# Kernel optimization log

Measured on AMD Instinct MI355X. Metric: run time of the kernel, lower is better.

Reference implementation:

```python
import jax, jax.numpy as jnp
import numpy as np


def setup_inputs() -> dict:
    key = jax.random.key(0)
    k1, k2, k3, k4 = jax.random.split(key, 4)
    B, Q, D, H = 8, 512, 4096, 1024
    return {
        "query_embeddings": jax.random.normal(k1, (B, Q, H), dtype=jnp.float32),
        "document_embeddings": jax.random.normal(k2, (B, D, H), dtype=jnp.float32),
        "attention_mask": jax.random.randint(k3, (B, D), 0, 2, dtype=jnp.int32),
        "proj_w": jax.random.normal(k4, (H, H), dtype=jnp.float32) * (H ** -0.5),
        "proj_b": jnp.zeros((H,), dtype=jnp.float32),
    }


def reference(query_embeddings, document_embeddings, attention_mask, proj_w, proj_b):
    H = query_embeddings.shape[-1]
    scale = 1.0 / jnp.sqrt(jnp.asarray(H, dtype=query_embeddings.dtype))
    # Linear projection of queries: [B, Q, H]
    q = jnp.einsum("bqh,hk->bqk", query_embeddings, proj_w) + proj_b
    # Scores: [B, Q, D]
    scores = jnp.einsum("bqh,bdh->bqd", q, document_embeddings) * scale
    # Mask: [B, 1, D]; masked positions -> -inf before softmax
    mask = attention_mask[:, None, :] != 0
    scores = jnp.where(mask, scores, -jnp.inf)
    attention_weights = jax.nn.softmax(scores, axis=-1)
    # Weighted sum over docs: [B, Q, H]
    retrieved_docs = jnp.einsum("bqd,bdh->bqh", attention_weights, document_embeddings)
    return (retrieved_docs, attention_weights)
```

## Files before the change

### kernel.cpp

```cpp
#include <hip/hip_runtime.h>

#define BATCH 8
#define QLEN 512
#define DLEN 4096
#define HDIM 1024

typedef __attribute__((ext_vector_type(8))) short bf16x8;
typedef __attribute__((ext_vector_type(4))) float f32x4;
typedef __attribute__((ext_vector_type(4))) short s16x4;

__device__ __forceinline__ short f2bf(float f) {
    union { float f; unsigned u; } x; x.f = f;
    unsigned r = x.u + 0x7fffu + ((x.u >> 16) & 1u);
    return (short)(r >> 16);
}

__device__ __forceinline__ void gload_lds16(const void* g, void* l) {
    __builtin_amdgcn_global_load_lds(
        (const __attribute__((address_space(1))) unsigned int*)g,
        (__attribute__((address_space(3))) unsigned int*)l,
        16, 0, 0);
}

__global__ void cvt_f32_bf16(const float* __restrict__ in, short* __restrict__ out, int n4) {
    int i = blockIdx.x * blockDim.x + threadIdx.x;
    int stride = gridDim.x * blockDim.x;
    for (; i < n4; i += stride) {
        float4 x = ((const float4*)in)[i];
        s16x4 o = { f2bf(x.x), f2bf(x.y), f2bf(x.z), f2bf(x.w) };
        ((s16x4*)out)[i] = o;
    }
}

__global__ void transpose_w(const float* __restrict__ W, short* __restrict__ Wt) {
    __shared__ float t[32][33];
    const int hb = blockIdx.y * 32, kb = blockIdx.x * 32;
    #pragma unroll
    for (int i = 0; i < 4; ++i) {
        int h = threadIdx.y + i * 8;
        t[h][threadIdx.x] = W[(size_t)(hb + h) * HDIM + kb + threadIdx.x];
    }
    __syncthreads();
    #pragma unroll
    for (int i = 0; i < 4; ++i) {
        int k = threadIdx.y + i * 8;
        Wt[(size_t)(kb + k) * HDIM + hb + threadIdx.x] = f2bf(t[threadIdx.x][k]);
    }
}

__global__ void transpose_docs(const short* __restrict__ docsB, short* __restrict__ docsT) {
    __shared__ unsigned t[64][65];
    const int b = blockIdx.z;
    const int h0 = blockIdx.x * 64, d0 = blockIdx.y * 64;
    const int tq = threadIdx.x & 15;
    const int tr = threadIdx.x >> 4;
    #pragma unroll
    for (int i = 0; i < 4; ++i) {
        int d = tr + i * 16;
        s16x4 v = *(const s16x4*)(docsB + ((size_t)b * DLEN + d0 + d) * HDIM + h0 + tq * 4);
        t[d][tq * 4 + 0] = (unsigned short)v[0];
        t[d][tq * 4 + 1] = (unsigned short)v[1];
        t[d][tq * 4 + 2] = (unsigned short)v[2];
        t[d][tq * 4 + 3] = (unsigned short)v[3];
    }
    __syncthreads();
    #pragma unroll
    for (int i = 0; i < 4; ++i) {
        int h = tr + i * 16;
        s16x4 o = { (short)t[tq * 4 + 0][h], (short)t[tq * 4 + 1][h],
                    (short)t[tq * 4 + 2][h], (short)t[tq * 4 + 3][h] };
        *(s16x4*)(docsT + ((size_t)b * HDIM + h0 + h) * DLEN + d0 + tq * 4) = o;
    }
}

#define BM 128
#define BN 128
#define BK 64
#define TILE_SH (BM * BK)

template<int EPI>
__global__ void gemm_bt(const short* __restrict__ A, const short* __restrict__ B,
                        void* __restrict__ Cv, const float* __restrict__ bias,
                        float scale, int N, int Kstride, int Kloop, int kOffStep,
                        int sx, int sxy,
                        long long aB, long long bB, long long cB) {
    __shared__ short As[2 * TILE_SH];
    __shared__ short Bs[2 * TILE_SH];
    const int tid  = threadIdx.x;
    const int lane = tid & 63;
    const int wv   = tid >> 6;
    const int wr   = wv >> 1, wc = wv & 1;

    const int wg = (blockIdx.x & 7) * (gridDim.x >> 3) + (blockIdx.x >> 3);
    const int bx = wg & ((1 << sx) - 1);
    const int by = (wg >> sx) & ((1 << (sxy - sx)) - 1);
    const int z  = wg >> sxy;

    const size_t rowBase = (size_t)by * BM;
    const size_t colBase = (size_t)bx * BN;
    const int bb = z & 7;
    const int kOff = (z >> 3) * kOffStep;
    const short* Ag = A + (size_t)bb * aB + kOff;
    const short* Bg = B + (size_t)bb * bB + kOff;

    f32x4 acc[4][4];
    #pragma unroll
    for (int m = 0; m < 4; ++m)
        #pragma unroll
        for (int n = 0; n < 4; ++n)
            acc[m][n] = (f32x4){0.f, 0.f, 0.f, 0.f};

    const short* aSrc[4]; const short* bSrc[4]; int dOff[4];
    #pragma unroll
    for (int i = 0; i < 4; ++i) {
        const int c = tid + 256 * i;
        const int r = c >> 3, cc = c & 7;
        const int gk = (cc ^ (r & 7)) << 3;
        aSrc[i] = Ag + (rowBase + r) * (size_t)Kstride + gk;
        bSrc[i] = Bg + (colBase + r) * (size_t)Kstride + gk;
        dOff[i] = c * 8;
    }
    const int lr = lane & 15;
    const int lk = (lane >> 4) << 3;

    const int nt = Kloop / BK;

    #pragma unroll
    for (int i = 0; i < 4; ++i) gload_lds16(aSrc[i], As + dOff[i]);
    #pragma unroll
    for (int i = 0; i < 4; ++i) gload_lds16(bSrc[i], Bs + dOff[i]);
    __syncthreads();

    int cur = 0;
    for (int t = 0; t < nt; ++t) {
        if (t + 1 < nt) {
            const int kt = (t + 1) * BK;
            const int o = (cur ^ 1) * TILE_SH;
            #pragma unroll
            for (int i = 0; i < 4; ++i) gload_lds16(aSrc[i] + kt, As + o + dOff[i]);
            #pragma unroll
            for (int i = 0; i < 4; ++i) gload_lds16(bSrc[i] + kt, Bs + o + dOff[i]);
        }

        const short* Ab = As + cur * TILE_SH;
        const short* Bb = Bs + cur * TILE_SH;
        #pragma unroll
        for (int kk = 0; kk < 2; ++kk) {
            const int chunkL = (kk * 32 + lk) >> 3;
            bf16x8 af[4], bfr[4];
            #pragma unroll
            for (int m = 0; m < 4; ++m) {
                const int row = wr * 64 + m * 16 + lr;
                af[m] = *(const bf16x8*)(Ab + row * BK + ((chunkL ^ (row & 7)) << 3));
            }
            #pragma unroll
            for (int n = 0; n < 4; ++n) {
                const int row = wc * 64 + n * 16 + lr;
                bfr[n] = *(const bf16x8*)(Bb + row * BK + ((chunkL ^ (row & 7)) << 3));
            }
            #pragma unroll
            for (int m = 0; m < 4; ++m)
                #pragma unroll
                for (int n = 0; n < 4; ++n)
                    acc[m][n] = __builtin_amdgcn_mfma_f32_16x16x32_bf16(af[m], bfr[n], acc[m][n], 0, 0, 0);
        }
        __syncthreads();
        cur ^= 1;
    }

    const int orow = (lane >> 4) << 2;
    const int ocol = lane & 15;
    #pragma unroll
    for (int n = 0; n < 4; ++n) {
        const size_t col = colBase + wc * 64 + n * 16 + ocol;
        const float bv = (EPI == 0) ? bias[col] : 0.f;
        #pragma unroll
        for (int m = 0; m < 4; ++m) {
            const size_t rbase = rowBase + wr * 64 + m * 16 + orow;
            #pragma unroll
            for (int j = 0; j < 4; ++j) {
                const float v = acc[m][n][j];
                const size_t off = (size_t)z * cB + (rbase + j) * (size_t)N + col;
                if (EPI == 0)      ((short*)Cv)[off] = f2bf(v + bv);
                else if (EPI == 1) ((float*)Cv)[off] = v * scale;
                else               ((float*)Cv)[off] = v;
            }
        }
    }
}

__global__ void reduce4(const float* __restrict__ p, float* __restrict__ out, int n4) {
    int i = blockIdx.x * blockDim.x + threadIdx.x;
    const int stride = gridDim.x * blockDim.x;
    const float4* p4 = (const float4*)p;
    float4* o4 = (float4*)out;
    for (; i < n4; i += stride) {
        float4 a = p4[i];
        float4 b = p4[i + 1048576];
        float4 c = p4[i + 2097152];
        float4 d = p4[i + 3145728];
        float4 r;
        r.x = a.x + b.x + c.x + d.x;
        r.y = a.y + b.y + c.y + d.y;
        r.z = a.z + b.z + c.z + d.z;
        r.w = a.w + b.w + c.w + d.w;
        o4[i] = r;
    }
}

__global__ void softmax_rows(const float* __restrict__ scores, const int* __restrict__ mask,
                             float* __restrict__ attnF, short* __restrict__ attnB) {
    const int row = blockIdx.x;
    const int b   = row >> 9;
    const int tid = threadIdx.x;
    const int lane = tid & 63;
    const int wv = tid >> 6;
    const float4* S  = (const float4*)(scores + (size_t)row * DLEN);
    const int4*   Mk = (const int4*)(mask + (size_t)b * DLEN);
    __shared__ float red[8];

    float v[16];
    float mx = -INFINITY;
    #pragma unroll
    for (int i = 0; i < 4; ++i) {
        float4 s = S[i * 256 + tid];
        int4   m = Mk[i * 256 + tid];
        v[i * 4 + 0] = m.x ? s.x : -INFINITY;
        v[i * 4 + 1] = m.y ? s.y : -INFINITY;
        v[i * 4 + 2] = m.z ? s.z : -INFINITY;
        v[i * 4 + 3] = m.w ? s.w : -INFINITY;
        #pragma unroll
        for (int c = 0; c < 4; ++c) mx = fmaxf(mx, v[i * 4 + c]);
    }
    #pragma unroll
    for (int o = 32; o > 0; o >>= 1) mx = fmaxf(mx, __shfl_xor(mx, o));
    if (lane == 0) red[wv] = mx;
    __syncthreads();
    mx = fmaxf(fmaxf(red[0], red[1]), fmaxf(red[2], red[3]));

    float sum = 0.f;
    #pragma unroll
    for (int i = 0; i < 16; ++i) {
        float e = __expf(v[i] - mx);
        v[i] = e;
        sum += e;
    }
    #pragma unroll
    for (int o = 32; o > 0; o >>= 1) sum += __shfl_xor(sum, o);
    __syncthreads();
    if (lane == 0) red[4 + wv] = sum;
    __syncthreads();
    sum = red[4] + red[5] + red[6] + red[7];
    const float inv = 1.0f / sum;

    float4* OF = (float4*)(attnF + (size_t)row * DLEN);
    s16x4*  OB = (s16x4*)(attnB + (size_t)row * DLEN);
    #pragma unroll
    for (int i = 0; i < 4; ++i) {
        float4 w;
        w.x = v[i * 4 + 0] * inv;
        w.y = v[i * 4 + 1] * inv;
        w.z = v[i * 4 + 2] * inv;
        w.w = v[i * 4 + 3] * inv;
        OF[i * 256 + tid] = w;
        s16x4 o = { f2bf(w.x), f2bf(w.y), f2bf(w.z), f2bf(w.w) };
        OB[i * 256 + tid] = o;
    }
}

extern "C" void kernel_launch(void* const* d_in, const int* in_sizes, int n_in,
                              void* d_out, int out_size, void* d_ws, size_t ws_size,
                              hipStream_t stream) {
    const float* qe   = (const float*)d_in[0];
    const float* docs = (const float*)d_in[1];
    const int*   mask = (const int*)d_in[2];
    const float* pw   = (const float*)d_in[3];
    const float* pb   = (const float*)d_in[4];

    float* outRet  = (float*)d_out;
    float* outAttn = outRet + (size_t)BATCH * QLEN * HDIM;

    char* ws = (char*)d_ws;
    short* qeB   = (short*)(ws + 0);
    short* wt    = (short*)(ws + 8388608);
    short* qpB   = (short*)(ws + 10485760);
    short* docsB = (short*)(ws + 18874368);
    short* docsT = (short*)(ws + 85983232);
    float* scor  = (float*)(ws + 153092096);
    short* attnB = (short*)(ws + 220200960);

    cvt_f32_bf16<<<dim3(1024), dim3(256), 0, stream>>>(qe, qeB, (BATCH * QLEN * HDIM) / 4);
    cvt_f32_bf16<<<dim3(2048), dim3(256), 0, stream>>>(docs, docsB, (BATCH * DLEN * HDIM) / 4);
    transpose_w<<<dim3(32, 32), dim3(32, 8), 0, stream>>>(pw, wt);
    transpose_docs<<<dim3(HDIM / 64, DLEN / 64, BATCH), dim3(256), 0, stream>>>(docsB, docsT);

    gemm_bt<0><<<dim3(256), dim3(256), 0, stream>>>(
        qeB, wt, (void*)qpB, pb, 1.f, HDIM, HDIM, HDIM, 0, 3, 8,
        0LL, 0LL, 0LL);

    gemm_bt<1><<<dim3(1024), dim3(256), 0, stream>>>(
        qpB, docsB, (void*)scor, nullptr, 0.03125f, DLEN, HDIM, HDIM, 0, 5, 7,
        (long long)QLEN * HDIM, (long long)DLEN * HDIM, (long long)QLEN * DLEN);

    softmax_rows<<<dim3(BATCH * QLEN), dim3(256), 0, stream>>>(scor, mask, outAttn, attnB);

    gemm_bt<2><<<dim3(1024), dim3(256), 0, stream>>>(
        attnB, docsT, (void*)scor, nullptr, 1.f, HDIM, DLEN, DLEN / 4, DLEN / 4, 3, 5,
        (long long)QLEN * DLEN, (long long)HDIM * DLEN, (long long)QLEN * HDIM);

    reduce4<<<dim3(2048), dim3(256), 0, stream>>>(scor, outRet, (BATCH * QLEN * HDIM) / 4);
}
```

Before: 421.4 us.

## Triple-buffer GEMM LDS tiles with BK=32 and vmcnt-based partial waits

Halves the K tile to 32 and uses three LDS buffers so loads run two tiles ahead of compute. The full __syncthreads drain is replaced by explicit s_waitcnt vmcnt partial waits plus a raw s_barrier, with a new swizzle for the 4-chunk row layout. This aims to overlap global-to-LDS loads with MFMA work better and cut barrier stalls. The cost is twice as many loop iterations and barriers per K, less MFMA work per barrier, and reliance on correct vmcnt accounting. Dropping the LDS wait from the barrier may also risk reads racing the global_load_lds writes.

```diff
diff --git a/kernel.cpp b/kernel.cpp
--- a/kernel.cpp
+++ b/kernel.cpp
@@ -21,6 +21,8 @@
         (__attribute__((address_space(3))) unsigned int*)l,
         16, 0, 0);
 }
+
+#define WAIT_VMCNT(n) asm volatile("s_waitcnt vmcnt(" #n ")" ::: "memory")
 
 __global__ void cvt_f32_bf16(const float* __restrict__ in, short* __restrict__ out, int n4) {
     int i = blockIdx.x * blockDim.x + threadIdx.x;
@@ -75,7 +77,7 @@
 
 #define BM 128
 #define BN 128
-#define BK 64
+#define BK 32
 #define TILE_SH (BM * BK)
 
 template<int EPI>
@@ -84,8 +86,8 @@
                         float scale, int N, int Kstride, int Kloop, int kOffStep,
                         int sx, int sxy,
                         long long aB, long long bB, long long cB) {
-    __shared__ short As[2 * TILE_SH];
-    __shared__ short Bs[2 * TILE_SH];
+    __shared__ short As[3 * TILE_SH];
+    __shared__ short Bs[3 * TILE_SH];
     const int tid  = threadIdx.x;
     const int lane = tid & 63;
     const int wv   = tid >> 6;
@@ -110,62 +112,68 @@
         for (int n = 0; n < 4; ++n)
             acc[m][n] = (f32x4){0.f, 0.f, 0.f, 0.f};
 
-    const short* aSrc[4]; const short* bSrc[4]; int dOff[4];
-    #pragma unroll
-    for (int i = 0; i < 4; ++i) {
+    const short* aSrc[2]; const short* bSrc[2]; int dOff[2];
+    #pragma unroll
+    for (int i = 0; i < 2; ++i) {
         const int c = tid + 256 * i;
-        const int r = c >> 3, cc = c & 7;
-        const int gk = (cc ^ (r & 7)) << 3;
+        const int r = c >> 2, cc = c & 3;
+        const int gk = (cc ^ ((r >> 1) & 3)) << 3;
         aSrc[i] = Ag + (rowBase + r) * (size_t)Kstride + gk;
         bSrc[i] = Bg + (colBase + r) * (size_t)Kstride + gk;
         dOff[i] = c * 8;
     }
+    const int chunkL = lane >> 4;
     const int lr = lane & 15;
-    const int lk = (lane >> 4) << 3;
 
     const int nt = Kloop / BK;
 
     #pragma unroll
-    for (int i = 0; i < 4; ++i) gload_lds16(aSrc[i], As + dOff[i]);
-    #pragma unroll
-    for (int i = 0; i < 4; ++i) gload_lds16(bSrc[i], Bs + dOff[i]);
-    __syncthreads();
-
-    int cur = 0;
+    for (int i = 0; i < 2; ++i) gload_lds16(aSrc[i], As + dOff[i]);
+    #pragma unroll
+    for (int i = 0; i < 2; ++i) gload_lds16(bSrc[i], Bs + dOff[i]);
+    #pragma unroll
+    for (int i = 0; i < 2; ++i) gload_lds16(aSrc[i] + BK, As + TILE_SH + dOff[i]);
+    #pragma unroll
+    for (int i = 0; i < 2; ++i) gload_lds16(bSrc[i] + BK, Bs + TILE_SH + dOff[i]);
+    WAIT_VMCNT(4);
+    __builtin_amdgcn_s_barrier();
+
     for (int t = 0; t < nt; ++t) {
+        if (t + 2 < nt) {
+            const int kt = (t + 2) * BK;
+            const int o = ((t + 2) % 3) * TILE_SH;
+            #pragma unroll
+            for (int i = 0; i < 2; ++i) gload_lds16(aSrc[i] + kt, As + o + dOff[i]);
+            #pragma unroll
+            for (int i = 0; i < 2; ++i) gload_lds16(bSrc[i] + kt, Bs + o + dOff[i]);
+        }
+
+        const short* Ab = As + (t % 3) * TILE_SH;
+        const short* Bb = Bs + (t % 3) * TILE_SH;
+        bf16x8 af[4], bfr[4];
+        #pragma unroll
+        for (int m = 0; m < 4; ++m) {
+            const int row = wr * 64 + m * 16 + lr;
+            af[m] = *(const bf16x8*)(Ab + row * BK + ((chunkL ^ ((row >> 1) & 3)) << 3));
+        }
+        #pragma unroll
+        for (int n = 0; n < 4; ++n) {
+            const int row = wc * 64 + n * 16 + lr;
+            bfr[n] = *(const bf16x8*)(Bb + row * BK + ((chunkL ^ ((row >> 1) & 3)) << 3));
+        }
+        #pragma unroll
+        for (int m = 0; m < 4; ++m)
+            #pragma unroll
+            for (int n = 0; n < 4; ++n)
+                acc[m][n] = __builtin_amdgcn_mfma_f32_16x16x32_bf16(af[m], bfr[n], acc[m][n], 0, 0, 0);
+
         if (t + 1 < nt) {
-            const int kt = (t + 1) * BK;
-            const int o = (cur ^ 1) * TILE_SH;
-            #pragma unroll
-            for (int i = 0; i < 4; ++i) gload_lds16(aSrc[i] + kt, As + o + dOff[i]);
-            #pragma unroll
-            for (int i = 0; i < 4; ++i) gload_lds16(bSrc[i] + kt, Bs + o + dOff[i]);
-        }
-
-        const short* Ab = As + cur * TILE_SH;
-        const short* Bb = Bs + cur * TILE_SH;
-        #pragma unroll
-        for (int kk = 0; kk < 2; ++kk) {
-            const int chunkL = (kk * 32 + lk) >> 3;
-            bf16x8 af[4], bfr[4];
-            #pragma unroll
-            for (int m = 0; m < 4; ++m) {
-                const int row = wr * 64 + m * 16 + lr;
-                af[m] = *(const bf16x8*)(Ab + row * BK + ((chunkL ^ (row & 7)) << 3));
-            }
-            #pragma unroll
-            for (int n = 0; n < 4; ++n) {
-                const int row = wc * 64 + n * 16 + lr;
-                bfr[n] = *(const bf16x8*)(Bb + row * BK + ((chunkL ^ (row & 7)) << 3));
-            }
-            #pragma unroll
-            for (int m = 0; m < 4; ++m)
-                #pragma unroll
-                for (int n = 0; n < 4; ++n)
-                    acc[m][n] = __builtin_amdgcn_mfma_f32_16x16x32_bf16(af[m], bfr[n], acc[m][n], 0, 0, 0);
-        }
-        __syncthreads();
-        cur ^= 1;
+            if (t + 2 < nt) { WAIT_VMCNT(4); }
+            else           { WAIT_VMCNT(0); }
+            __builtin_amdgcn_sched_barrier(0);
+            __builtin_amdgcn_s_barrier();
+            __builtin_amdgcn_sched_barrier(0);
+        }
     }
 
     const int orow = (lane >> 4) << 2;
```

After: 452.3 us. 7.3% more time.
